# Kernel tuning notes

Measured on AMD Instinct MI355X. Metric: run time of the kernel, lower is better.

## Reference

```python
import jax, jax.numpy as jnp
import numpy as np


def setup_inputs() -> dict:
    key = jax.random.key(0)
    k1, k2 = jax.random.split(key)
    B, C, H, W = 32, 256, 64, 64
    data = jax.random.normal(k1, (B, C, H, W), dtype=jnp.float32)
    offset = jax.random.normal(k2, (B, 2, H, W), dtype=jnp.float32)
    trans_std = jnp.float32(0.005)  # learned scalar Parameter
    return {"data": data, "offset": offset, "trans_std": trans_std}


def reference(data, offset, trans_std):
    """Offset-driven bilinear interpolation sampling + global average pooling.

    data:   [B, C, H, W]
    offset: [B, 2, H, W]  (dy, dx) displacement field, scaled by trans_std
    Returns pooled features [B, C].
    """
    B, C, H, W = data.shape
    ts = jnp.clip(trans_std, 0.001, 0.01)  # forward clamps trans_std to [0.001, 0.01]

    # sampling coordinates: base grid + scaled offsets (offsets normalized by H/W)
    ii = jnp.arange(H, dtype=data.dtype)[:, None]   # [H,1]
    jj = jnp.arange(W, dtype=data.dtype)[None, :]   # [1,W]
    y = jnp.clip(ii + ts * offset[:, 0] * H, 0.0, H - 1)  # [B,H,W]
    x = jnp.clip(jj + ts * offset[:, 1] * W, 0.0, W - 1)  # [B,H,W]

    y0 = jnp.clip(jnp.floor(y).astype(jnp.int32), 0, H - 2)
    x0 = jnp.clip(jnp.floor(x).astype(jnp.int32), 0, W - 2)
    y1 = y0 + 1
    x1 = x0 + 1
    wy = y - y0.astype(data.dtype)  # [B,H,W] in [0,1]
    wx = x - x0.astype(data.dtype)

    def sample_one(d, yy0, yy1, xx0, xx1):
        # d: [C,H,W]; index maps: [H,W] -> gathered [C,H,W]
        v00 = d[:, yy0, xx0]
        v01 = d[:, yy0, xx1]
        v10 = d[:, yy1, xx0]
        v11 = d[:, yy1, xx1]
        return v00, v01, v10, v11

    v00, v01, v10, v11 = jax.vmap(sample_one)(data, y0, y1, x0, x1)  # each [B,C,H,W]

    wy_ = wy[:, None]  # broadcast over channels -> [B,1,H,W]
    wx_ = wx[:, None]
    sampled = ((1 - wy_) * (1 - wx_) * v00 + (1 - wy_) * wx_ * v01
               + wy_ * (1 - wx_) * v10 + wy_ * wx_ * v11)  # [B,C,H,W]

    # pooling: global average over spatial locations -> [B,C]
    return jnp.mean(sampled, axis=(2, 3))
```

## Files before the change

### kernel.cpp

```cpp
#include <hip/hip_runtime.h>

#define BATCH 32
#define CHAN  256
#define HGT   64
#define WID   64
#define HW    4096

__global__ __launch_bounds__(1024) void weight_map_kernel(
        const float* __restrict__ offset,
        const float* __restrict__ ts_ptr,
        float* __restrict__ A)
{
    const int b   = blockIdx.x;
    const int tid = threadIdx.x;

    __shared__ float acc[HW];
    acc[tid]        = 0.0f;
    acc[tid + 1024] = 0.0f;
    acc[tid + 2048] = 0.0f;
    acc[tid + 3072] = 0.0f;
    __syncthreads();

    float ts = ts_ptr[0];
    ts = fminf(fmaxf(ts, 0.001f), 0.01f);

    const float* off_y = offset + (size_t)b * 2 * HW;
    const float* off_x = off_y + HW;

    #pragma unroll
    for (int it = 0; it < 4; ++it) {
        const int p = tid + it * 1024;
        const int i = p >> 6;
        const int j = p & 63;
        const float dy = off_y[p];
        const float dx = off_x[p];
        float y = fminf(fmaxf((float)i + ts * dy * 64.0f, 0.0f), 63.0f);
        float x = fminf(fmaxf((float)j + ts * dx * 64.0f, 0.0f), 63.0f);
        int y0 = (int)floorf(y); y0 = min(max(y0, 0), HGT - 2);
        int x0 = (int)floorf(x); x0 = min(max(x0, 0), WID - 2);
        const float wy = y - (float)y0;
        const float wx = x - (float)x0;
        const int base = (y0 << 6) + x0;
        atomicAdd(&acc[base],           (1.0f - wy) * (1.0f - wx));
        atomicAdd(&acc[base + 1],       (1.0f - wy) * wx);
        atomicAdd(&acc[base + WID],     wy * (1.0f - wx));
        atomicAdd(&acc[base + WID + 1], wy * wx);
    }
    __syncthreads();

    float* Ab = A + (size_t)b * HW;
    const float s = 1.0f / (float)HW;
    Ab[tid]        = acc[tid]        * s;
    Ab[tid + 1024] = acc[tid + 1024] * s;
    Ab[tid + 2048] = acc[tid + 2048] * s;
    Ab[tid + 3072] = acc[tid + 3072] * s;
}

__global__ __launch_bounds__(256, 4) void dot_kernel(
        const float* __restrict__ data,
        const float* __restrict__ A,
        float* __restrict__ out)
{
    const int blk = blockIdx.x;
    const int b   = blk >> 6;
    const int tid = threadIdx.x;
    const int w   = tid >> 6;
    const int lane = tid & 63;

    __shared__ __align__(16) float As[HW];

    {
        const float* Ab = A + (size_t)b * HW;
        #pragma unroll
        for (int s = 0; s < 4; ++s) {
            const int idx = (s * 256 + tid) * 4;
            *reinterpret_cast<float4*>(As + idx) =
                *reinterpret_cast<const float4*>(Ab + idx);
        }
    }
    __syncthreads();

    const float* plane = data + (size_t)(blk * 4 + w) * HW;

    float4 d[16];
    #pragma unroll
    for (int s = 0; s < 16; ++s)
        d[s] = *reinterpret_cast<const float4*>(plane + s * 256 + lane * 4);

    float a0 = 0.0f, a1 = 0.0f, a2 = 0.0f, a3 = 0.0f;
    #pragma unroll
    for (int s = 0; s < 16; ++s) {
        const float4 av = *reinterpret_cast<const float4*>(As + s * 256 + lane * 4);
        if ((s & 3) == 0) {
            a0 = fmaf(av.x, d[s].x, a0); a0 = fmaf(av.y, d[s].y, a0);
            a0 = fmaf(av.z, d[s].z, a0); a0 = fmaf(av.w, d[s].w, a0);
        } else if ((s & 3) == 1) {
            a1 = fmaf(av.x, d[s].x, a1); a1 = fmaf(av.y, d[s].y, a1);
            a1 = fmaf(av.z, d[s].z, a1); a1 = fmaf(av.w, d[s].w, a1);
        } else if ((s & 3) == 2) {
            a2 = fmaf(av.x, d[s].x, a2); a2 = fmaf(av.y, d[s].y, a2);
            a2 = fmaf(av.z, d[s].z, a2); a2 = fmaf(av.w, d[s].w, a2);
        } else {
            a3 = fmaf(av.x, d[s].x, a3); a3 = fmaf(av.y, d[s].y, a3);
            a3 = fmaf(av.z, d[s].z, a3); a3 = fmaf(av.w, d[s].w, a3);
        }
    }
    float sum = (a0 + a1) + (a2 + a3);

    #pragma unroll
    for (int off = 32; off > 0; off >>= 1)
        sum += __shfl_down(sum, off, 64);

    if (lane == 0) out[blk * 4 + w] = sum;
}

extern "C" void kernel_launch(void* const* d_in, const int* in_sizes, int n_in,
                              void* d_out, int out_size, void* d_ws, size_t ws_size,
                              hipStream_t stream) {
    const float* data   = (const float*)d_in[0];
    const float* offset = (const float*)d_in[1];
    const float* ts     = (const float*)d_in[2];

    float* A   = (float*)d_ws;
    float* out = (float*)d_out;

    weight_map_kernel<<<BATCH, 1024, 0, stream>>>(offset, ts, A);
    dot_kernel<<<(BATCH * CHAN) / 4, 256, 0, stream>>>(data, A, out);
}
```

Before: 212.5 us.

## Fuse weight-map construction into the pooling dot kernel, recomputing per block

Merges the two launches into one kernel. Each 1024-thread block handles 16 channels of one batch, rebuilds that batch's bilinear weight map in shared memory with atomics, and then dots it with the channel planes it loaded earlier. This removes the global round trip for the weight map and one kernel launch. The weight map is now rebuilt 16 times per batch instead of once, and each block carries 64 float4 registers per thread at 1024 threads, so register pressure and occupancy may suffer.

```diff
diff --git a/kernel.cpp b/kernel.cpp
--- a/kernel.cpp
+++ b/kernel.cpp
@@ -5,92 +5,70 @@
 #define HGT   64
 #define WID   64
 #define HW    4096
+#define CPB   16
 
-__global__ __launch_bounds__(1024) void weight_map_kernel(
+__global__ __launch_bounds__(1024, 4) void fused_bilinear_pool(
+        const float* __restrict__ data,
         const float* __restrict__ offset,
         const float* __restrict__ ts_ptr,
-        float* __restrict__ A)
+        float* __restrict__ out)
 {
-    const int b   = blockIdx.x;
-    const int tid = threadIdx.x;
+    const int blk  = blockIdx.x;
+    const int b    = blk >> 4;
+    const int g    = blk & 15;
+    const int tid  = threadIdx.x;
+    const int w    = tid >> 6;
+    const int lane = tid & 63;
 
     __shared__ float acc[HW];
+
     acc[tid]        = 0.0f;
     acc[tid + 1024] = 0.0f;
     acc[tid + 2048] = 0.0f;
     acc[tid + 3072] = 0.0f;
     __syncthreads();
 
-    float ts = ts_ptr[0];
-    ts = fminf(fmaxf(ts, 0.001f), 0.01f);
-
     const float* off_y = offset + (size_t)b * 2 * HW;
     const float* off_x = off_y + HW;
+    const float4 dy4 = *reinterpret_cast<const float4*>(off_y + tid * 4);
+    const float4 dx4 = *reinterpret_cast<const float4*>(off_x + tid * 4);
 
-    #pragma unroll
-    for (int it = 0; it < 4; ++it) {
-        const int p = tid + it * 1024;
-        const int i = p >> 6;
-        const int j = p & 63;
-        const float dy = off_y[p];
-        const float dx = off_x[p];
-        float y = fminf(fmaxf((float)i + ts * dy * 64.0f, 0.0f), 63.0f);
-        float x = fminf(fmaxf((float)j + ts * dx * 64.0f, 0.0f), 63.0f);
-        int y0 = (int)floorf(y); y0 = min(max(y0, 0), HGT - 2);
-        int x0 = (int)floorf(x); x0 = min(max(x0, 0), WID - 2);
-        const float wy = y - (float)y0;
-        const float wx = x - (float)x0;
-        const int base = (y0 << 6) + x0;
-        atomicAdd(&acc[base],           (1.0f - wy) * (1.0f - wx));
-        atomicAdd(&acc[base + 1],       (1.0f - wy) * wx);
-        atomicAdd(&acc[base + WID],     wy * (1.0f - wx));
-        atomicAdd(&acc[base + WID + 1], wy * wx);
-    }
-    __syncthreads();
-
-    float* Ab = A + (size_t)b * HW;
-    const float s = 1.0f / (float)HW;
-    Ab[tid]        = acc[tid]        * s;
-    Ab[tid + 1024] = acc[tid + 1024] * s;
-    Ab[tid + 2048] = acc[tid + 2048] * s;
-    Ab[tid + 3072] = acc[tid + 3072] * s;
-}
-
-__global__ __launch_bounds__(256, 4) void dot_kernel(
-        const float* __restrict__ data,
-        const float* __restrict__ A,
-        float* __restrict__ out)
-{
-    const int blk = blockIdx.x;
-    const int b   = blk >> 6;
-    const int tid = threadIdx.x;
-    const int w   = tid >> 6;
-    const int lane = tid & 63;
-
-    __shared__ __align__(16) float As[HW];
-
-    {
-        const float* Ab = A + (size_t)b * HW;
-        #pragma unroll
-        for (int s = 0; s < 4; ++s) {
-            const int idx = (s * 256 + tid) * 4;
-            *reinterpret_cast<float4*>(As + idx) =
-                *reinterpret_cast<const float4*>(Ab + idx);
-        }
-    }
-    __syncthreads();
-
-    const float* plane = data + (size_t)(blk * 4 + w) * HW;
-
+    const float* plane = data + ((size_t)(b * CHAN + g * CPB + w)) * HW;
     float4 d[16];
     #pragma unroll
     for (int s = 0; s < 16; ++s)
         d[s] = *reinterpret_cast<const float4*>(plane + s * 256 + lane * 4);
 
+    float ts = ts_ptr[0];
+    ts = fminf(fmaxf(ts, 0.001f), 0.01f);
+
+    {
+        const int i  = tid >> 4;
+        const int j0 = (tid << 2) & 63;
+        const float dys[4] = {dy4.x, dy4.y, dy4.z, dy4.w};
+        const float dxs[4] = {dx4.x, dx4.y, dx4.z, dx4.w};
+        #pragma unroll
+        for (int e = 0; e < 4; ++e) {
+            float y = fminf(fmaxf((float)i        + ts * dys[e] * 64.0f, 0.0f), 63.0f);
+            float x = fminf(fmaxf((float)(j0 + e) + ts * dxs[e] * 64.0f, 0.0f), 63.0f);
+            int y0 = (int)floorf(y); y0 = min(max(y0, 0), HGT - 2);
+            int x0 = (int)floorf(x); x0 = min(max(x0, 0), WID - 2);
+            const float wy = y - (float)y0;
+            const float wx = x - (float)x0;
+            const int base = (y0 << 6) + x0;
+            atomicAdd(&acc[base],           (1.0f - wy) * (1.0f - wx));
+            atomicAdd(&acc[base + 1],       (1.0f - wy) * wx);
+            atomicAdd(&acc[base + WID],     wy * (1.0f - wx));
+            atomicAdd(&acc[base + WID + 1], wy * wx);
+        }
+    }
+    __syncthreads();
+
     float a0 = 0.0f, a1 = 0.0f, a2 = 0.0f, a3 = 0.0f;
     #pragma unroll
     for (int s = 0; s < 16; ++s) {
-        const float4 av = *reinterpret_cast<const float4*>(As + s * 256 + lane * 4);
+        const float4 av =
+            *reinterpret_cast<const float4*>(acc + s * 256 + lane * 4);
         if ((s & 3) == 0) {
             a0 = fmaf(av.x, d[s].x, a0); a0 = fmaf(av.y, d[s].y, a0);
             a0 = fmaf(av.z, d[s].z, a0); a0 = fmaf(av.w, d[s].w, a0);
@@ -111,7 +89,8 @@
     for (int off = 32; off > 0; off >>= 1)
         sum += __shfl_down(sum, off, 64);
 
-    if (lane == 0) out[blk * 4 + w] = sum;
+    if (lane == 0)
+        out[(b << 8) + g * CPB + w] = sum * (1.0f / (float)HW);
 }
 
 extern "C" void kernel_launch(void* const* d_in, const int* in_sizes, int n_in,
@@ -121,9 +100,8 @@
     const float* offset = (const float*)d_in[1];
     const float* ts     = (const float*)d_in[2];
 
-    float* A   = (float*)d_ws;
     float* out = (float*)d_out;
+    (void)d_ws; (void)ws_size;
 
-    weight_map_kernel<<<BATCH, 1024, 0, stream>>>(offset, ts, A);
-    dot_kernel<<<(BATCH * CHAN) / 4, 256, 0, stream>>>(data, A, out);
+    fused_bilinear_pool<<<BATCH * CPB, 1024, 0, stream>>>(data, offset, ts, out);
 }
```

Result: faster. 204.1 us (-4.0%).
